# Optimization experiments

Hardware: AMD Instinct MI355X
Metric: run time of the kernel (lower is better)

The kernel has to match this reference:

```python
import jax, jax.numpy as jnp
import numpy as np

H = 512        # hidden_size
ENC = 2 * H    # encoder (context) feature dim
V = 10000      # vocab_size
B, T, L = 32, 500, 100
NEG_INF = -1e10


def setup_inputs() -> dict:
    key = jax.random.key(0)
    ks = jax.random.split(key, 16)
    sc = 0.02
    inp = {
        "h_batch": jax.random.normal(ks[0], (B, T, ENC), jnp.float32),
        "seq_lens": jax.random.randint(ks[1], (B,), 1, T + 1),
        "labels": jax.random.randint(ks[2], (B, L), 0, V),
        # content-based (additive) attention params
        "attn_Ws": jax.random.normal(ks[3], (H, H), jnp.float32) * sc,
        "attn_Wh": jax.random.normal(ks[4], (ENC, H), jnp.float32) * sc,
        "attn_b": jnp.zeros((H,), jnp.float32),
        "attn_v": jax.random.normal(ks[5], (H,), jnp.float32) * sc,
        # output path
        "W_sy": jax.random.normal(ks[6], (H, H), jnp.float32) * sc,
        "b_sy": jnp.zeros((H,), jnp.float32),
        "W_gy": jax.random.normal(ks[7], (ENC, H), jnp.float32) * sc,
        "b_gy": jnp.zeros((H,), jnp.float32),
        "W_yy": jax.random.normal(ks[8], (H, V), jnp.float32) * sc,
        "b_yy": jnp.zeros((V,), jnp.float32),
        # recurrence path
        "E_yr": jax.random.normal(ks[9], (V, 4 * H), jnp.float32) * sc,
        "W_sr": jax.random.normal(ks[10], (H, 4 * H), jnp.float32) * sc,
        "b_sr": jnp.zeros((4 * H,), jnp.float32),
        "W_gr": jax.random.normal(ks[11], (ENC, 4 * H), jnp.float32) * sc,
        "b_gr": jnp.zeros((4 * H,), jnp.float32),
    }
    return inp


def _func_lstm(rec_in, c):
    i, f, g, o = jnp.split(rec_in, 4, axis=-1)
    c_new = jax.nn.sigmoid(f) * c + jax.nn.sigmoid(i) * jnp.tanh(g)
    s_new = jax.nn.sigmoid(o) * jnp.tanh(c_new)
    return s_new, c_new


def reference(h_batch, seq_lens, labels, attn_Ws, attn_Wh, attn_b, attn_v,
              W_sy, b_sy, W_gy, b_gy, W_yy, b_yy,
              E_yr, W_sr, b_sr, W_gr, b_gr):
    Tlen = h_batch.shape[1]
    mask = jnp.arange(Tlen)[None, :] < seq_lens[:, None]          # [B,T]
    h_proj = jnp.einsum('bte,eh->bth', h_batch, attn_Wh) + attn_b  # precompute

    s0 = jnp.zeros((h_batch.shape[0], H), h_batch.dtype)
    c0 = jnp.zeros_like(s0)

    def step(carry, y_t):
        s, c = carry
        # content-based attention: e = v . tanh(Ws s + Wh h)
        e = jnp.einsum('bth,h->bt', jnp.tanh(h_proj + (s @ attn_Ws)[:, None, :]), attn_v)
        e = jnp.where(mask, e, NEG_INF)
        alpha = jax.nn.softmax(e, axis=-1)                         # [B,T]
        g = jnp.einsum('bt,bte->be', alpha, h_batch)               # [B,ENC]
        dec_feat = (g @ W_gy + b_gy) + (s @ W_sy + b_sy)
        y = jnp.tanh(dec_feat) @ W_yy + b_yy                       # [B,V]
        rec_in = E_yr[y_t] + (s @ W_sr + b_sr) + (g @ W_gr + b_gr) # [B,4H]
        s_new, c_new = _func_lstm(rec_in, c)
        return (s_new, c_new), y

    _, preds = jax.lax.scan(step, (s0, c0), labels.T)              # [L,B,V]
    return jnp.transpose(preds, (1, 0, 2))                         # [B,L,V]
```

## Files before the change

kernel.cpp:

```cpp
#include <hip/hip_runtime.h>
#include <cstdint>

#define B_   32
#define T_   500
#define H_   512
#define ENC_ 1024
#define V_   10000
#define L_   100
#define H4_  2048
#define NB_  256
#define NT_  512

#define OFF_HPROJ 0
#define OFF_WYYP  4096000
#define OFF_WRECP 6656000
#define OFF_WSB   10588160
#define OFF_S     10719232
#define OFF_DECTP 10735616
#define OFF_RACC  10752000
#define OFF_G0    10817536
#define OFF_G1    10850304
#define OFF_E     10883072
#define OFF_DEN   10899456
#define OFF_BAR   10899520
#define OFF_HB16  10899584
#define ZERO_CNT  180352

using bf16x8 = __attribute__((ext_vector_type(8))) short;
using f32x4  = __attribute__((ext_vector_type(4))) float;

__device__ __forceinline__ f32x4 mfma16(bf16x8 a, bf16x8 b, f32x4 c){
  return __builtin_amdgcn_mfma_f32_16x16x32_bf16(a, b, c, 0, 0, 0);
}
__device__ __forceinline__ unsigned short bfr(float f){
  unsigned x = __float_as_uint(f);
  return (unsigned short)((x + 0x7FFFu + ((x>>16)&1u)) >> 16);
}
__device__ __forceinline__ void bfsplit(float f, short& hi, short& lo){
  unsigned short h = bfr(f);
  float hf = __uint_as_float(((unsigned)h) << 16);
  hi = (short)h;
  lo = (short)bfr(f - hf);
}
__device__ __forceinline__ float bf2f(unsigned short u){
  return __uint_as_float(((unsigned)u) << 16);
}
__device__ __forceinline__ float ftanh(float x){
  float t = fminf(fmaxf(2.f*x, -30.f), 30.f);
  float e = __expf(t);
  return (e - 1.f) / (e + 1.f);
}
__device__ __forceinline__ float fsig(float x){
  float t = fminf(fmaxf(x, -30.f), 30.f);
  return 1.f / (1.f + __expf(-t));
}
__device__ __forceinline__ float gload(const float* p){
  return __hip_atomic_load((float*)p, __ATOMIC_RELAXED, __HIP_MEMORY_SCOPE_AGENT);
}
__device__ __forceinline__ void gstore(float* p, float v){
  __hip_atomic_store(p, v, __ATOMIC_RELAXED, __HIP_MEMORY_SCOPE_AGENT);
}
__device__ __forceinline__ void gstoreu(unsigned* p, unsigned v){
  __hip_atomic_store(p, v, __ATOMIC_RELAXED, __HIP_MEMORY_SCOPE_AGENT);
}
__device__ __forceinline__ void gload2(const float* p, float& a, float& b){
  unsigned long long u = __hip_atomic_load((const unsigned long long*)p,
                          __ATOMIC_RELAXED, __HIP_MEMORY_SCOPE_AGENT);
  a = __uint_as_float((unsigned)u);
  b = __uint_as_float((unsigned)(u >> 32));
}
__device__ __forceinline__ void gloadu2(const unsigned* p, unsigned& a, unsigned& b){
  unsigned long long u = __hip_atomic_load((const unsigned long long*)p,
                          __ATOMIC_RELAXED, __HIP_MEMORY_SCOPE_AGENT);
  a = (unsigned)u;
  b = (unsigned)(u >> 32);
}

__device__ __forceinline__ void gridbar(unsigned* bars, unsigned it){
  asm volatile("s_waitcnt vmcnt(0) lgkmcnt(0)" ::: "memory");
  __syncthreads();
  if (threadIdx.x == 0){
    unsigned* gc = bars + 1 + (blockIdx.x & 15);
    unsigned old = __hip_atomic_fetch_add(gc, 1u, __ATOMIC_RELAXED, __HIP_MEMORY_SCOPE_AGENT);
    if (old == it*16u + 15u)
      __hip_atomic_fetch_add(bars, 1u, __ATOMIC_RELAXED, __HIP_MEMORY_SCOPE_AGENT);
    while (__hip_atomic_load(bars, __ATOMIC_RELAXED, __HIP_MEMORY_SCOPE_AGENT) < (it+1u)*16u)
      __builtin_amdgcn_s_sleep(2);
  }
  __syncthreads();
  asm volatile("" ::: "memory");
}

__global__ void k_init(float* __restrict__ ws){
  int i = blockIdx.x * 256 + threadIdx.x;
  if (i < ZERO_CNT) ws[OFF_S + i] = 0.f;
}

__global__ void k_packWyy(const float* __restrict__ Wyy, float* __restrict__ ws){
  unsigned short* wp = (unsigned short*)(ws + OFF_WYYP);
  int t = blockIdx.x * 256 + threadIdx.x;
  if (t >= 625*16*64) return;
  int vt = t / 1024;
  int rem = t - vt*1024;
  int kc = rem >> 6, lane = rem & 63;
  int v  = vt*16 + (lane & 15);
  int k0 = kc*32 + ((lane >> 4) << 3);
  bf16x8 H;
  #pragma unroll
  for (int j = 0; j < 8; ++j) H[j] = (short)bfr(Wyy[(size_t)(k0+j)*V_ + v]);
  *(bf16x8*)(wp + ((size_t)(vt*16 + kc)*64 + lane)*8) = H;
}

__global__ void k_packWrec(const float* __restrict__ Wsy, const float* __restrict__ Wgy,
                           const float* __restrict__ Wsr, const float* __restrict__ Wgr,
                           float* __restrict__ ws){
  unsigned short* wp = (unsigned short*)(ws + OFF_WRECP);
  int t = blockIdx.x * 256 + threadIdx.x;
  if (t >= 160*48*64) return;
  int vt = t / (48*64);
  int rem = t - vt*(48*64);
  int kc = rem >> 6, lane = rem & 63;
  int col = vt*16 + (lane & 15);
  int k0  = kc*32 + ((lane >> 4) << 3);
  bf16x8 H;
  #pragma unroll
  for (int j = 0; j < 8; ++j){
    int k = k0 + j;
    float x;
    if (k < 512) x = (col < 512) ? Wsy[(size_t)k*512 + col] : Wsr[(size_t)k*2048 + (col-512)];
    else         x = (col < 512) ? Wgy[(size_t)(k-512)*512 + col] : Wgr[(size_t)(k-512)*2048 + (col-512)];
    H[j] = (short)bfr(x);
  }
  *(bf16x8*)(wp + ((size_t)(vt*48 + kc)*64 + lane)*8) = H;
}

__global__ void k_packWs(const float* __restrict__ Ws, float* __restrict__ ws){
  unsigned short* wp = (unsigned short*)(ws + OFF_WSB);
  int i = blockIdx.x * 256 + threadIdx.x;
  wp[i] = bfr(Ws[i]);
}

__global__ void k_packHB(const float* __restrict__ hb, float* __restrict__ ws){
  unsigned short* wp = (unsigned short*)(ws + OFF_HB16);
  int i = blockIdx.x * 256 + threadIdx.x;
  if (i < B_*T_*ENC_) wp[i] = bfr(hb[i]);
}

__global__ void k_hproj(const float* __restrict__ A, const float* __restrict__ W,
                        const float* __restrict__ bias, const int* __restrict__ lens,
                        float* __restrict__ ws){
  unsigned short* C = (unsigned short*)(ws + OFF_HPROJ);
  const int bm = blockIdx.x * 64;
  const int bn = blockIdx.y * 64;
  {
    int b0 = bm / T_, t0 = bm % T_;
    int b1 = (bm + 63) / T_;
    if (b0 == b1 && t0 >= lens[b0]) return;
  }
  __shared__ float As[64][33];
  __shared__ float Bs[32][68];
  const int tid = threadIdx.x;
  const int tx = tid & 15, ty = tid >> 4;
  float acc[4][4];
  #pragma unroll
  for (int i = 0; i < 4; ++i)
    #pragma unroll
    for (int j = 0; j < 4; ++j) acc[i][j] = 0.f;
  for (int k0 = 0; k0 < 1024; k0 += 32){
    for (int i = tid; i < 64*32; i += 256){
      int rr = i >> 5, cc = i & 31;
      As[rr][cc] = A[(size_t)(bm + rr) * 1024 + k0 + cc];
    }
    for (int i = tid; i < 32*64; i += 256){
      int rr = i >> 6, cc = i & 63;
      Bs[rr][cc] = W[(size_t)(k0 + rr) * 512 + bn + cc];
    }
    __syncthreads();
    #pragma unroll
    for (int kk = 0; kk < 32; ++kk){
      float a0 = As[ty*4+0][kk], a1 = As[ty*4+1][kk];
      float a2 = As[ty*4+2][kk], a3 = As[ty*4+3][kk];
      float4 b4 = *(const float4*)&Bs[kk][tx*4];
      acc[0][0] += a0*b4.x; acc[0][1] += a0*b4.y; acc[0][2] += a0*b4.z; acc[0][3] += a0*b4.w;
      acc[1][0] += a1*b4.x; acc[1][1] += a1*b4.y; acc[1][2] += a1*b4.z; acc[1][3] += a1*b4.w;
      acc[2][0] += a2*b4.x; acc[2][1] += a2*b4.y; acc[2][2] += a2*b4.z; acc[2][3] += a2*b4.w;
      acc[3][0] += a3*b4.x; acc[3][1] += a3*b4.y; acc[3][2] += a3*b4.z; acc[3][3] += a3*b4.w;
    }
    __syncthreads();
  }
  #pragma unroll
  for (int i = 0; i < 4; ++i){
    int m = bm + ty*4 + i;
    ushort4 o;
    o.x = bfr(acc[i][0] + bias[bn + tx*4 + 0]);
    o.y = bfr(acc[i][1] + bias[bn + tx*4 + 1]);
    o.z = bfr(acc[i][2] + bias[bn + tx*4 + 2]);
    o.w = bfr(acc[i][3] + bias[bn + tx*4 + 3]);
    *(ushort4*)&C[(size_t)m * 512 + bn + tx*4] = o;
  }
}

__global__ __launch_bounds__(NT_, 2) void k_persist(
    const int* __restrict__ lens,
    const int* __restrict__ labels, const float* __restrict__ av,
    const float* __restrict__ bsy, const float* __restrict__ bgy,
    const float* __restrict__ byy,
    const float* __restrict__ Eyr,
    const float* __restrict__ bsr, const float* __restrict__ bgr,
    float* __restrict__ out, float* __restrict__ ws)
{
  const int blk = blockIdx.x;
  const int tid = threadIdx.x;
  const int w   = tid >> 6;
  const int lane= tid & 63;
  unsigned* bars = (unsigned*)(ws + OFF_BAR);
  const unsigned short* wyyp  = (const unsigned short*)(ws + OFF_WYYP);
  const unsigned short* wrecp = (const unsigned short*)(ws + OFF_WRECP);
  const unsigned short* wsb   = (const unsigned short*)(ws + OFF_WSB);
  const unsigned short* hpB   = (const unsigned short*)(ws + OFF_HPROJ);
  const unsigned short* hb16  = (const unsigned short*)(ws + OFF_HB16);
  unsigned* dectP = (unsigned*)(ws + OFF_DECTP);
  unsigned* sP    = (unsigned*)(ws + OFF_S);
  __shared__ __align__(16) float smem[18688];

  const int arow  = lane & 15;
  const int klane = (lane >> 4) << 3;
  float c_reg = 0.f;

  for (int l = 0; l <= L_; ++l){
    const int p = l & 1;
    const int goff = p ? OFF_G1 : OFF_G0;
    if (blk < 157){
      if (l > 0){
        unsigned* dst = (unsigned*)smem;
        for (int i = tid; i < 8192; i += NT_){
          int row = i >> 8, k2 = (i & 255) << 1;
          unsigned a, b;
          gloadu2(dectP + row*H_ + k2, a, b);
          dst[row*516 + k2]     = a;
          dst[row*516 + k2 + 1] = b;
        }
        __syncthreads();
        const int kh = w & 1;
        const int vtslot = w >> 1;
        const int vt = blk*4 + vtslot;
        f32x4 a0 = {0.f,0.f,0.f,0.f}, a1 = {0.f,0.f,0.f,0.f};
        if (vt < 625){
          for (int kc2 = 0; kc2 < 8; ++kc2){
            const int kc = kh*8 + kc2;
            const int k0 = kc*32 + klane;
            bf16x8 Ahi0, Alo0, Ahi1, Alo1;
            {
              const unsigned* dp = dst + arow*516 + k0;
              uint4 qa = *(const uint4*)(dp);
              uint4 qb = *(const uint4*)(dp+4);
              unsigned q[8] = {qa.x,qa.y,qa.z,qa.w,qb.x,qb.y,qb.z,qb.w};
              #pragma unroll
              for (int j = 0; j < 8; ++j){
                Ahi0[j] = (short)(q[j] >> 16);
                Alo0[j] = (short)(q[j] & 0xFFFFu);
              }
            }
            {
              const unsigned* dp = dst + (arow+16)*516 + k0;
              uint4 qa = *(const uint4*)(dp);
              uint4 qb = *(const uint4*)(dp+4);
              unsigned q[8] = {qa.x,qa.y,qa.z,qa.w,qb.x,qb.y,qb.z,qb.w};
              #pragma unroll
              for (int j = 0; j < 8; ++j){
                Ahi1[j] = (short)(q[j] >> 16);
                Alo1[j] = (short)(q[j] & 0xFFFFu);
              }
            }
            bf16x8 Bv = *(const bf16x8*)(wyyp + ((size_t)(vt*16 + kc)*64 + lane)*8);
            a0 = mfma16(Ahi0, Bv, a0);
            a0 = mfma16(Alo0, Bv, a0);
            a1 = mfma16(Ahi1, Bv, a1);
            a1 = mfma16(Alo1, Bv, a1);
          }
        }
        float* red = smem + 16512;
        if (vt < 625 && kh == 0){
          #pragma unroll
          for (int r = 0; r < 4; ++r){
            red[vtslot*512 +       lane*4 + r] = a0[r];
            red[vtslot*512 + 256 + lane*4 + r] = a1[r];
          }
        }
        __syncthreads();
        if (vt < 625 && kh == 1){
          const int v = vt*16 + arow;
          const float bv = byy[v];
          const int lv = l - 1;
          #pragma unroll
          for (int r = 0; r < 4; ++r){
            const int row0 = ((lane >> 4) << 2) + r;
            float v0 = red[vtslot*512 +       lane*4 + r] + a0[r] + bv;
            float v1 = red[vtslot*512 + 256 + lane*4 + r] + a1[r] + bv;
            out[((size_t)(row0)*L_      + lv)*V_ + v] = v0;
            out[((size_t)(row0 + 16)*L_ + lv)*V_ + v] = v1;
          }
        }
        __syncthreads();
      }
    } else if (blk < 221){
      if (l < L_){
        const int u = blk - 157;
        const int b = u >> 1, half = u & 1;
        float* ssm = smem;
        float* part = smem + 512;
        float* wsm = smem + 2560;
        if (l == 0){
          ssm[tid] = 0.f;
          c_reg = 0.f;
        } else {
          const int h = tid;
          const float* ey = Eyr + (size_t)labels[b*L_ + (l-1)] * H4_;
          float ri = gload(&ws[OFF_RACC + b*H4_ + h])        + bsr[h]      + bgr[h]      + ey[h];
          float rf = gload(&ws[OFF_RACC + b*H4_ + 512 + h])  + bsr[512+h]  + bgr[512+h]  + ey[512+h];
          float rg = gload(&ws[OFF_RACC + b*H4_ + 1024 + h]) + bsr[1024+h] + bgr[1024+h] + ey[1024+h];
          float ro = gload(&ws[OFF_RACC + b*H4_ + 1536 + h]) + bsr[1536+h] + bgr[1536+h] + ey[1536+h];
          float cn = fsig(rf)*c_reg + fsig(ri)*ftanh(rg);
          float sn = fsig(ro)*ftanh(cn);
          c_reg = cn;
          if (half == 0){
            short h_, lo_; bfsplit(sn, h_, lo_);
            gstoreu(&sP[b*H_ + h], ((unsigned)(unsigned short)h_ << 16) | (unsigned short)(unsigned short)lo_);
          }
          ssm[h] = sn;
        }
        __syncthreads();
        {
          const int colp = tid & 255;
          const int kh2  = tid >> 8;
          const int col0 = colp*2;
          const float* sp = ssm + kh2*256;
          const unsigned short* wb = wsb + (size_t)(kh2*256)*512 + col0;
          float acc0 = 0.f, acc1 = 0.f;
          for (int k = 0; k < 256; k += 8){
            float4 s0 = *(const float4*)&sp[k];
            float4 s1 = *(const float4*)&sp[k+4];
            unsigned wv[8];
            #pragma unroll
            for (int j = 0; j < 8; ++j)
              wv[j] = *(const unsigned*)&wb[(size_t)(k+j)*512];
            float sv[8] = {s0.x,s0.y,s0.z,s0.w,s1.x,s1.y,s1.z,s1.w};
            #pragma unroll
            for (int j = 0; j < 8; ++j){
              acc0 += sv[j] * bf2f((unsigned short)(wv[j] & 0xFFFFu));
              acc1 += sv[j] * bf2f((unsigned short)(wv[j] >> 16));
            }
          }
          part[kh2*1024 + col0]     = acc0;
          part[kh2*1024 + col0 + 1] = acc1;
        }
        __syncthreads();
        wsm[tid] = part[tid] + part[1024 + tid];
        __syncthreads();
        const int len = lens[b];
        float avr[8], swr[8];
        #pragma unroll
        for (int j = 0; j < 8; ++j){
          avr[j] = av[lane*8 + j];
          swr[j] = wsm[lane*8 + j];
        }
        float* e = ws + OFF_E;
        for (int t = 2*w + half; t < len; t += 16){
          bf16x8 hp = *(const bf16x8*)&hpB[(size_t)(b*T_ + t)*512 + lane*8];
          float sum = 0.f;
          #pragma unroll
          for (int j = 0; j < 8; ++j)
            sum += avr[j] * ftanh(bf2f((unsigned short)hp[j]) + swr[j]);
          #pragma unroll
          for (int off = 32; off > 0; off >>= 1) sum += __shfl_xor(sum, off, 64);
          if (lane == 0) gstore(&e[b*T_ + t], __expf(sum));
        }
      }
    } else {
      if (l < L_){
        for (int i = (blk - 221)*NT_ + tid; i < B_*ENC_; i += 35*NT_)
          gstore(&ws[goff + i], 0.f);
        if (blk == 221 && tid < 32)
          gstore(&ws[OFF_DEN + p*32 + tid], 0.f);
      }
    }
    if (l == L_) break;
    gridbar(bars, (unsigned)(l*3 + 0));

    {
      const int b = blk >> 3, ts = blk & 7;
      const int len = lens[b];
      const int clen = (len + 7) >> 3;
      const int t0 = ts*clen;
      const int t1 = min(t0 + clen, len);
      const int n  = t1 - t0;
      float* sc = smem;
      float* pg = smem + 128;
      if (tid < n) sc[tid] = gload(&ws[OFF_E + b*T_ + t0 + tid]);
      __syncthreads();
      if (n > 0 && tid < 64){
        float s2 = 0.f;
        for (int i = tid; i < n; i += 64) s2 += sc[i];
        #pragma unroll
        for (int off = 32; off > 0; off >>= 1) s2 += __shfl_xor(s2, off, 64);
        if (tid == 0) atomicAdd(&ws[OFF_DEN + p*32 + b], s2);
      }
      const int tg = tid >> 8, cq = tid & 255;
      const int col0 = cq*4;
      {
        float4 acc = {0.f,0.f,0.f,0.f};
        const unsigned short* hp = hb16 + (size_t)b*T_*ENC_ + col0;
        for (int t = t0 + tg; t < t1; t += 2){
          ushort4 x = *(const ushort4*)&hp[(size_t)t * ENC_];
          float a = sc[t - t0];
          acc.x += a*bf2f(x.x); acc.y += a*bf2f(x.y);
          acc.z += a*bf2f(x.z); acc.w += a*bf2f(x.w);
        }
        *(float4*)&pg[tg*1024 + col0] = acc;
      }
      __syncthreads();
      if (tg == 0 && n > 0){
        float4 x0 = *(const float4*)&pg[col0];
        float4 x1 = *(const float4*)&pg[1024 + col0];
        float* gp = ws + goff + b*ENC_ + col0;
        atomicAdd(gp+0, x0.x+x1.x);
        atomicAdd(gp+1, x0.y+x1.y);
        atomicAdd(gp+2, x0.z+x1.z);
        atomicAdd(gp+3, x0.w+x1.w);
      }
    }
    gridbar(bars, (unsigned)(l*3 + 1));

    if (blk < 80){
      const float invb0 = 1.f / gload(&ws[OFF_DEN + p*32 + arow]);
      const float invb1 = 1.f / gload(&ws[OFF_DEN + p*32 + arow + 16]);
      f32x4 acc[2][2];
      #pragma unroll
      for (int vv = 0; vv < 2; ++vv)
        #pragma unroll
        for (int rg = 0; rg < 2; ++rg) acc[vv][rg] = (f32x4){0.f,0.f,0.f,0.f};
      for (int j6 = 0; j6 < 6; ++j6){
        const int kc = w*6 + j6;
        const int k0 = kc*32 + klane;
        const bool isg = (k0 >= 512);
        bf16x8 Ahi0, Alo0, Ahi1, Alo1;
        if (!isg){
          unsigned q[8];
          const unsigned* dp = sP + arow*H_ + k0;
          gloadu2(dp+0, q[0], q[1]);
          gloadu2(dp+2, q[2], q[3]);
          gloadu2(dp+4, q[4], q[5]);
          gloadu2(dp+6, q[6], q[7]);
          #pragma unroll
          for (int j = 0; j < 8; ++j){
            Ahi0[j] = (short)(q[j] >> 16);
            Alo0[j] = (short)(q[j] & 0xFFFFu);
          }
          const unsigned* dp1 = sP + (arow+16)*H_ + k0;
          gloadu2(dp1+0, q[0], q[1]);
          gloadu2(dp1+2, q[2], q[3]);
          gloadu2(dp1+4, q[4], q[5]);
          gloadu2(dp1+6, q[6], q[7]);
          #pragma unroll
          for (int j = 0; j < 8; ++j){
            Ahi1[j] = (short)(q[j] >> 16);
            Alo1[j] = (short)(q[j] & 0xFFFFu);
          }
        } else {
          {
            const float* src = &ws[goff + arow*ENC_ + (k0 - 512)];
            float x[8];
            gload2(src+0, x[0], x[1]);
            gload2(src+2, x[2], x[3]);
            gload2(src+4, x[4], x[5]);
            gload2(src+6, x[6], x[7]);
            #pragma unroll
            for (int j = 0; j < 8; ++j){
              short h, lo; bfsplit(x[j]*invb0, h, lo);
              Ahi0[j] = h; Alo0[j] = lo;
            }
          }
          {
            const float* src = &ws[goff + (arow+16)*ENC_ + (k0 - 512)];
            float x[8];
            gload2(src+0, x[0], x[1]);
            gload2(src+2, x[2], x[3]);
            gload2(src+4, x[4], x[5]);
            gload2(src+6, x[6], x[7]);
            #pragma unroll
            for (int j = 0; j < 8; ++j){
              short h, lo; bfsplit(x[j]*invb1, h, lo);
              Ahi1[j] = h; Alo1[j] = lo;
            }
          }
        }
        #pragma unroll
        for (int vv = 0; vv < 2; ++vv){
          const int vt = blk*2 + vv;
          bf16x8 Bv = *(const bf16x8*)(wrecp + ((size_t)(vt*48 + kc)*64 + lane)*8);
          acc[vv][0] = mfma16(Ahi0, Bv, acc[vv][0]);
          acc[vv][0] = mfma16(Alo0, Bv, acc[vv][0]);
          acc[vv][1] = mfma16(Ahi1, Bv, acc[vv][1]);
          acc[vv][1] = mfma16(Alo1, Bv, acc[vv][1]);
        }
      }
      #pragma unroll
      for (int vv = 0; vv < 2; ++vv)
        #pragma unroll
        for (int rg = 0; rg < 2; ++rg)
          #pragma unroll
          for (int r = 0; r < 4; ++r)
            smem[((w*2 + vv)*2 + rg)*256 + lane*4 + r] = acc[vv][rg][r];
      __syncthreads();
      #pragma unroll
      for (int oo = 0; oo < 2; ++oo){
        const int q   = tid + oo*512;
        const int vv  = q >> 9;
        const int rem = q & 511;
        const int bt  = rem >> 8;
        const int r8  = rem & 255;
        float v = 0.f;
        #pragma unroll
        for (int w8 = 0; w8 < 8; ++w8)
          v += smem[((w8*2 + vv)*2 + bt)*256 + r8];
        const int ln = r8 >> 2, rr = r8 & 3;
        const int row = bt*16 + ((ln >> 4) << 2) + rr;
        const int col = (blk*2 + vv)*16 + (ln & 15);
        if (col < 512){
          float t = ftanh(v + bsy[col] + bgy[col]);
          unsigned short hi_ = bfr(t);
          unsigned short lo_ = bfr(t - bf2f(hi_));
          gstoreu(&dectP[row*H_ + col], ((unsigned)hi_ << 16) | lo_);
        } else {
          gstore(&ws[OFF_RACC + row*H4_ + (col - 512)], v);
        }
      }
    }
    gridbar(bars, (unsigned)(l*3 + 2));
  }
}

extern "C" void kernel_launch(void* const* d_in, const int* in_sizes, int n_in,
                              void* d_out, int out_size, void* d_ws, size_t ws_size,
                              hipStream_t stream){
  const float* h_batch = (const float*)d_in[0];
  const int*   seq_lens= (const int*)d_in[1];
  const int*   labels  = (const int*)d_in[2];
  const float* attn_Ws = (const float*)d_in[3];
  const float* attn_Wh = (const float*)d_in[4];
  const float* attn_b  = (const float*)d_in[5];
  const float* attn_v  = (const float*)d_in[6];
  const float* W_sy    = (const float*)d_in[7];
  const float* b_sy    = (const float*)d_in[8];
  const float* W_gy    = (const float*)d_in[9];
  const float* b_gy    = (const float*)d_in[10];
  const float* W_yy    = (const float*)d_in[11];
  const float* b_yy    = (const float*)d_in[12];
  const float* E_yr    = (const float*)d_in[13];
  const float* W_sr    = (const float*)d_in[14];
  const float* b_sr    = (const float*)d_in[15];
  const float* W_gr    = (const float*)d_in[16];
  const float* b_gr    = (const float*)d_in[17];
  float* out = (float*)d_out;
  float* ws  = (float*)d_ws;

  k_init    <<<705, 256, 0, stream>>>(ws);
  k_packWyy <<<2500, 256, 0, stream>>>(W_yy, ws);
  k_packWrec<<<1920, 256, 0, stream>>>(W_sy, W_gy, W_sr, W_gr, ws);
  k_packWs  <<<1024, 256, 0, stream>>>(attn_Ws, ws);
  k_packHB  <<<64000, 256, 0, stream>>>(h_batch, ws);
  k_hproj   <<<dim3(250, 8), 256, 0, stream>>>(h_batch, attn_Wh, attn_b, seq_lens, ws);

  void* kargs[] = {
    (void*)&seq_lens, (void*)&labels, (void*)&attn_v,
    (void*)&b_sy, (void*)&b_gy, (void*)&b_yy,
    (void*)&E_yr, (void*)&b_sr, (void*)&b_gr,
    (void*)&out, (void*)&ws
  };
  hipLaunchCooperativeKernel((void*)k_persist, dim3(NB_), dim3(NT_), kargs, 0, stream);
}
```

Measured before the change: 9.647 ms.

## Fuse attention softmax-context into score blocks, drop one grid barrier per step

The score-computing blocks now keep exp(scores) in shared memory and compute the softmax denominator and the weighted context sum themselves. This removes the global score buffer and one of the three grid-wide barriers per decode step. The recurrence GEMM is spread over 160 blocks with one tile each instead of 80 blocks with two. Zeroing of the other ping-pong context buffer moves into the idle blocks of the GEMM phase. The trade-off is that the context reduction now runs on only 64 blocks, each streaming half a batch row's sequence, so that phase has less parallelism.

Measured after the change: 9.318 ms. 3.4% less time.

```diff
diff --git a/kernel.cpp b/kernel.cpp
--- a/kernel.cpp
+++ b/kernel.cpp
@@ -20,11 +20,10 @@
 #define OFF_RACC  10752000
 #define OFF_G0    10817536
 #define OFF_G1    10850304
-#define OFF_E     10883072
-#define OFF_DEN   10899456
-#define OFF_BAR   10899520
-#define OFF_HB16  10899584
-#define ZERO_CNT  180352
+#define OFF_DEN   10883072
+#define OFF_BAR   10883136
+#define OFF_HB16  10883200
+#define ZERO_CNT  163968
 
 using bf16x8 = __attribute__((ext_vector_type(8))) short;
 using f32x4  = __attribute__((ext_vector_type(4))) float;
@@ -307,9 +306,11 @@
       if (l < L_){
         const int u = blk - 157;
         const int b = u >> 1, half = u & 1;
-        float* ssm = smem;
+        float* ssm  = smem;
         float* part = smem + 512;
-        float* wsm = smem + 2560;
+        float* wsm  = smem + 2560;
+        float* ex   = smem + 3072;
+        float* pg   = smem + 3328;
         if (l == 0){
           ssm[tid] = 0.f;
           c_reg = 0.f;
@@ -325,7 +326,7 @@
           c_reg = cn;
           if (half == 0){
             short h_, lo_; bfsplit(sn, h_, lo_);
-            gstoreu(&sP[b*H_ + h], ((unsigned)(unsigned short)h_ << 16) | (unsigned short)(unsigned short)lo_);
+            gstoreu(&sP[b*H_ + h], ((unsigned)(unsigned short)h_ << 16) | (unsigned)(unsigned short)lo_);
           }
           ssm[h] = sn;
         }
@@ -358,87 +359,68 @@
         wsm[tid] = part[tid] + part[1024 + tid];
         __syncthreads();
         const int len = lens[b];
-        float avr[8], swr[8];
-        #pragma unroll
-        for (int j = 0; j < 8; ++j){
-          avr[j] = av[lane*8 + j];
-          swr[j] = wsm[lane*8 + j];
-        }
-        float* e = ws + OFF_E;
-        for (int t = 2*w + half; t < len; t += 16){
-          bf16x8 hp = *(const bf16x8*)&hpB[(size_t)(b*T_ + t)*512 + lane*8];
-          float sum = 0.f;
-          #pragma unroll
-          for (int j = 0; j < 8; ++j)
-            sum += avr[j] * ftanh(bf2f((unsigned short)hp[j]) + swr[j]);
-          #pragma unroll
-          for (int off = 32; off > 0; off >>= 1) sum += __shfl_xor(sum, off, 64);
-          if (lane == 0) gstore(&e[b*T_ + t], __expf(sum));
-        }
-      }
-    } else {
-      if (l < L_){
-        for (int i = (blk - 221)*NT_ + tid; i < B_*ENC_; i += 35*NT_)
-          gstore(&ws[goff + i], 0.f);
-        if (blk == 221 && tid < 32)
-          gstore(&ws[OFF_DEN + p*32 + tid], 0.f);
+        {
+          float avr[8], swr[8];
+          #pragma unroll
+          for (int j = 0; j < 8; ++j){
+            avr[j] = av[lane*8 + j];
+            swr[j] = wsm[lane*8 + j];
+          }
+          for (int t = 2*w + half; t < len; t += 16){
+            bf16x8 hp = *(const bf16x8*)&hpB[(size_t)(b*T_ + t)*512 + lane*8];
+            float sum = 0.f;
+            #pragma unroll
+            for (int j = 0; j < 8; ++j)
+              sum += avr[j] * ftanh(bf2f((unsigned short)hp[j]) + swr[j]);
+            #pragma unroll
+            for (int off = 32; off > 0; off >>= 1) sum += __shfl_xor(sum, off, 64);
+            if (lane == 0) ex[(t - half) >> 1] = __expf(sum);
+          }
+        }
+        __syncthreads();
+        const int n = (len - half + 1) >> 1;
+        if (tid < 64){
+          float s2 = 0.f;
+          for (int i = tid; i < n; i += 64) s2 += ex[i];
+          #pragma unroll
+          for (int off = 32; off > 0; off >>= 1) s2 += __shfl_xor(s2, off, 64);
+          if (tid == 0 && n > 0) atomicAdd(&ws[OFF_DEN + p*32 + b], s2);
+        }
+        {
+          const int tg = tid >> 7;
+          const int cl = tid & 127;
+          const int col0 = cl*8;
+          const unsigned short* hp = hb16 + (size_t)b*T_*ENC_ + col0;
+          float acc[8] = {0.f,0.f,0.f,0.f,0.f,0.f,0.f,0.f};
+          for (int idx = tg; idx < n; idx += 4){
+            const int t = half + 2*idx;
+            bf16x8 x = *(const bf16x8*)&hp[(size_t)t * ENC_];
+            float a = ex[idx];
+            #pragma unroll
+            for (int j = 0; j < 8; ++j) acc[j] += a * bf2f((unsigned short)x[j]);
+          }
+          *(float4*)&pg[tg*1024 + col0]     = *(float4*)&acc[0];
+          *(float4*)&pg[tg*1024 + col0 + 4] = *(float4*)&acc[4];
+        }
+        __syncthreads();
+        if (tid < 256 && n > 0){
+          const int c0 = tid*4;
+          #pragma unroll
+          for (int j = 0; j < 4; ++j){
+            float s = pg[c0+j] + pg[1024+c0+j] + pg[2048+c0+j] + pg[3072+c0+j];
+            atomicAdd(&ws[goff + b*ENC_ + c0 + j], s);
+          }
+        }
       }
     }
     if (l == L_) break;
-    gridbar(bars, (unsigned)(l*3 + 0));
-
-    {
-      const int b = blk >> 3, ts = blk & 7;
-      const int len = lens[b];
-      const int clen = (len + 7) >> 3;
-      const int t0 = ts*clen;
-      const int t1 = min(t0 + clen, len);
-      const int n  = t1 - t0;
-      float* sc = smem;
-      float* pg = smem + 128;
-      if (tid < n) sc[tid] = gload(&ws[OFF_E + b*T_ + t0 + tid]);
-      __syncthreads();
-      if (n > 0 && tid < 64){
-        float s2 = 0.f;
-        for (int i = tid; i < n; i += 64) s2 += sc[i];
-        #pragma unroll
-        for (int off = 32; off > 0; off >>= 1) s2 += __shfl_xor(s2, off, 64);
-        if (tid == 0) atomicAdd(&ws[OFF_DEN + p*32 + b], s2);
-      }
-      const int tg = tid >> 8, cq = tid & 255;
-      const int col0 = cq*4;
-      {
-        float4 acc = {0.f,0.f,0.f,0.f};
-        const unsigned short* hp = hb16 + (size_t)b*T_*ENC_ + col0;
-        for (int t = t0 + tg; t < t1; t += 2){
-          ushort4 x = *(const ushort4*)&hp[(size_t)t * ENC_];
-          float a = sc[t - t0];
-          acc.x += a*bf2f(x.x); acc.y += a*bf2f(x.y);
-          acc.z += a*bf2f(x.z); acc.w += a*bf2f(x.w);
-        }
-        *(float4*)&pg[tg*1024 + col0] = acc;
-      }
-      __syncthreads();
-      if (tg == 0 && n > 0){
-        float4 x0 = *(const float4*)&pg[col0];
-        float4 x1 = *(const float4*)&pg[1024 + col0];
-        float* gp = ws + goff + b*ENC_ + col0;
-        atomicAdd(gp+0, x0.x+x1.x);
-        atomicAdd(gp+1, x0.y+x1.y);
-        atomicAdd(gp+2, x0.z+x1.z);
-        atomicAdd(gp+3, x0.w+x1.w);
-      }
-    }
-    gridbar(bars, (unsigned)(l*3 + 1));
-
-    if (blk < 80){
+    gridbar(bars, (unsigned)(l*2 + 0));
+
+    if (blk < 160){
       const float invb0 = 1.f / gload(&ws[OFF_DEN + p*32 + arow]);
       const float invb1 = 1.f / gload(&ws[OFF_DEN + p*32 + arow + 16]);
-      f32x4 acc[2][2];
-      #pragma unroll
-      for (int vv = 0; vv < 2; ++vv)
-        #pragma unroll
-        for (int rg = 0; rg < 2; ++rg) acc[vv][rg] = (f32x4){0.f,0.f,0.f,0.f};
+      const int vt = blk;
+      f32x4 acc0 = {0.f,0.f,0.f,0.f}, acc1 = {0.f,0.f,0.f,0.f};
       for (int j6 = 0; j6 < 6; ++j6){
         const int kc = w*6 + j6;
         const int k0 = kc*32 + klane;
@@ -494,38 +476,27 @@
             }
           }
         }
-        #pragma unroll
-        for (int vv = 0; vv < 2; ++vv){
-          const int vt = blk*2 + vv;
-          bf16x8 Bv = *(const bf16x8*)(wrecp + ((size_t)(vt*48 + kc)*64 + lane)*8);
-          acc[vv][0] = mfma16(Ahi0, Bv, acc[vv][0]);
-          acc[vv][0] = mfma16(Alo0, Bv, acc[vv][0]);
-          acc[vv][1] = mfma16(Ahi1, Bv, acc[vv][1]);
-          acc[vv][1] = mfma16(Alo1, Bv, acc[vv][1]);
-        }
+        bf16x8 Bv = *(const bf16x8*)(wrecp + ((size_t)(vt*48 + kc)*64 + lane)*8);
+        acc0 = mfma16(Ahi0, Bv, acc0);
+        acc0 = mfma16(Alo0, Bv, acc0);
+        acc1 = mfma16(Ahi1, Bv, acc1);
+        acc1 = mfma16(Alo1, Bv, acc1);
       }
       #pragma unroll
-      for (int vv = 0; vv < 2; ++vv)
-        #pragma unroll
-        for (int rg = 0; rg < 2; ++rg)
-          #pragma unroll
-          for (int r = 0; r < 4; ++r)
-            smem[((w*2 + vv)*2 + rg)*256 + lane*4 + r] = acc[vv][rg][r];
+      for (int r = 0; r < 4; ++r){
+        smem[(w*2 + 0)*256 + lane*4 + r] = acc0[r];
+        smem[(w*2 + 1)*256 + lane*4 + r] = acc1[r];
+      }
       __syncthreads();
-      #pragma unroll
-      for (int oo = 0; oo < 2; ++oo){
-        const int q   = tid + oo*512;
-        const int vv  = q >> 9;
-        const int rem = q & 511;
-        const int bt  = rem >> 8;
-        const int r8  = rem & 255;
+      {
+        const int bt = tid >> 8, r8 = tid & 255;
         float v = 0.f;
         #pragma unroll
         for (int w8 = 0; w8 < 8; ++w8)
-          v += smem[((w8*2 + vv)*2 + bt)*256 + r8];
+          v += smem[(w8*2 + bt)*256 + r8];
         const int ln = r8 >> 2, rr = r8 & 3;
         const int row = bt*16 + ((ln >> 4) << 2) + rr;
-        const int col = (blk*2 + vv)*16 + (ln & 15);
+        const int col = blk*16 + (ln & 15);
         if (col < 512){
           float t = ftanh(v + bsy[col] + bgy[col]);
           unsigned short hi_ = bfr(t);
@@ -535,8 +506,14 @@
           gstore(&ws[OFF_RACC + row*H4_ + (col - 512)], v);
         }
       }
+    } else if (blk < 176){
+      const int zoff = p ? OFF_G0 : OFF_G1;
+      for (int i = (blk - 160)*NT_ + tid; i < B_*ENC_; i += 16*NT_)
+        gstore(&ws[zoff + i], 0.f);
+      if (blk == 160 && tid < 32)
+        gstore(&ws[OFF_DEN + (p^1)*32 + tid], 0.f);
     }
-    gridbar(bars, (unsigned)(l*3 + 2));
+    gridbar(bars, (unsigned)(l*2 + 1));
   }
 }
 
@@ -564,7 +541,7 @@
   float* out = (float*)d_out;
   float* ws  = (float*)d_ws;
 
-  k_init    <<<705, 256, 0, stream>>>(ws);
+  k_init    <<<641, 256, 0, stream>>>(ws);
   k_packWyy <<<2500, 256, 0, stream>>>(W_yy, ws);
   k_packWrec<<<1920, 256, 0, stream>>>(W_sy, W_gy, W_sr, W_gr, ws);
   k_packWs  <<<1024, 256, 0, stream>>>(attn_Ws, ws);
```
